# Performance work log

Hardware: AMD Instinct MI355X
Metric: run time of the kernel (lower is better)

Reference implementation:

```python
import jax, jax.numpy as jnp
import numpy as np

FG_THRESH = 0.5  # fg_iou_thresh in RetinaNetLoss.__init__
BG_THRESH = 0.4  # bg_iou_thresh
BELOW_LOW_QUALITY = -1
BETWEEN_THRESHOLDS = -2


def _make_boxes(key, lead_shape, img_size=800.0, max_wh=128.0):
    # Build valid xyxy boxes (x1<x2, y1<y2) inside an img_size image.
    k1, k2 = jax.random.split(key)
    cxcy = jax.random.uniform(k1, lead_shape + (2,), minval=0.0, maxval=img_size)
    wh = jax.random.uniform(k2, lead_shape + (2,), minval=8.0, maxval=max_wh)
    return jnp.concatenate([cxcy - wh * 0.5, cxcy + wh * 0.5], axis=-1)


def setup_inputs() -> dict:
    key = jax.random.key(0)
    kb, ka = jax.random.split(key)
    B, G, A = 8, 64, 120000
    gt_boxes = _make_boxes(kb, (B, G))                 # [B, G, 4] per-image gt boxes
    anchors = _make_boxes(ka, (A,), max_wh=256.0)      # [A, 4] shared anchors
    return {"gt_boxes": gt_boxes, "anchors": anchors}


def _box_iou(boxes1, boxes2):
    # boxes1 [G,4], boxes2 [A,4] -> IoU [G,A] (torchvision box_ops.box_iou)
    area1 = (boxes1[:, 2] - boxes1[:, 0]) * (boxes1[:, 3] - boxes1[:, 1])  # [G]
    area2 = (boxes2[:, 2] - boxes2[:, 0]) * (boxes2[:, 3] - boxes2[:, 1])  # [A]
    lt = jnp.maximum(boxes1[:, None, :2], boxes2[None, :, :2])  # [G,A,2]
    rb = jnp.minimum(boxes1[:, None, 2:], boxes2[None, :, 2:])  # [G,A,2]
    wh = jnp.clip(rb - lt, 0.0)
    inter = wh[..., 0] * wh[..., 1]  # [G,A]
    return inter / (area1[:, None] + area2[None, :] - inter)


def _match(quality):
    # torchvision Matcher(0.5, 0.4, allow_low_quality_matches=True) on quality [G,A]
    matched_vals = quality.max(axis=0)                      # [A] best IoU per anchor
    all_matches = jnp.argmax(quality, axis=0)               # [A] pre-threshold matches
    matches = jnp.where(matched_vals < BG_THRESH, BELOW_LOW_QUALITY, all_matches)
    matches = jnp.where((matched_vals >= BG_THRESH) & (matched_vals < FG_THRESH),
                        BETWEEN_THRESHOLDS, matches)
    # low-quality match recovery: anchors achieving the per-gt max keep their match
    highest_per_gt = quality.max(axis=1, keepdims=True)     # [G,1]
    pred_update = (quality == highest_per_gt).any(axis=0)   # [A]
    matches = jnp.where(pred_update, all_matches, matches)
    return matches.astype(jnp.int64), matched_vals


def reference(gt_boxes, anchors):
    # gt_boxes [B,G,4], anchors [A,4] -> matched_idxs [B,A] int64, matched_vals [B,A]
    def per_image(boxes):
        return _match(_box_iou(boxes, anchors))
    matched_idxs, matched_vals = jax.vmap(per_image)(gt_boxes)
    return matched_idxs, matched_vals
```

## Files before the change

kernel.cpp:

```cpp
#include <hip/hip_runtime.h>


static constexpr int G = 64;

__device__ __forceinline__ float opaque(float x) {
    asm volatile("" : "+v"(x));
    return x;
}

__device__ __forceinline__ int vindex(int i) {
    asm volatile("" : "+v"(i));
    return i;
}

__device__ __forceinline__ float box_area(float x1, float y1, float x2, float y2) {
    return opaque(__fmul_rn(__fsub_rn(x2, x1), __fsub_rn(y2, y1)));
}

__device__ __forceinline__ float inter_area(float gx1, float gy1, float gx2, float gy2,
                                            float ax1, float ay1, float ax2, float ay2) {
    float ltx = fmaxf(gx1, ax1);
    float lty = fmaxf(gy1, ay1);
    float rbx = fminf(gx2, ax2);
    float rby = fminf(gy2, ay2);
    float w = fmaxf(__fsub_rn(rbx, ltx), 0.0f);
    float h = fmaxf(__fsub_rn(rby, lty), 0.0f);
    return opaque(__fmul_rn(w, h));
}

__device__ __forceinline__ float div_rn(float n, float d) {
    float r = __builtin_amdgcn_rcpf(d);
    float e = fmaf(-d, r, 1.0f);
    r = fmaf(e, r, r);
    float q = __fmul_rn(n, r);
    float s = fmaf(-d, q, n);
    q = fmaf(s, r, q);
    s = fmaf(-d, q, n);
    q = fmaf(s, r, q);
    return q;
}

#define DPP_MAX_STAGE(x, ctrl)                                                   \
    do {                                                                         \
        int _yi = __builtin_amdgcn_update_dpp(__float_as_int(x),                 \
                                              __float_as_int(x), (ctrl),         \
                                              0xf, 0xf, false);                  \
        (x) = fmaxf((x), __int_as_float(_yi));                                   \
    } while (0)

__device__ __forceinline__ float wave_max_lane63(float x) {
    DPP_MAX_STAGE(x, 0xB1);
    DPP_MAX_STAGE(x, 0x4E);
    DPP_MAX_STAGE(x, 0x141);
    DPP_MAX_STAGE(x, 0x140);
    DPP_MAX_STAGE(x, 0x142);
    DPP_MAX_STAGE(x, 0x143);
    return x;
}

__global__ void k_init(const float* __restrict__ gt, unsigned int* __restrict__ hpg,
                       float* __restrict__ gab, int BG) {
    int i = blockIdx.x * 256 + threadIdx.x;
    if (i < BG) {
        hpg[i] = 0u;
        float4 gb = ((const float4*)gt)[i];
        gab[i] = box_area(gb.x, gb.y, gb.z, gb.w);
    }
}

template <bool STORE>
__global__ __launch_bounds__(256, 4)
void pass1_k(const float* __restrict__ gt,
             const float* __restrict__ anchors,
             const float* __restrict__ gab,
             unsigned int* __restrict__ hpg,
             unsigned int* __restrict__ sredg,
             float* __restrict__ vmaxA,
             int* __restrict__ amaxA,
             int A, int nchunks) {
    const int b = blockIdx.y;
    const int t = threadIdx.x;

    __shared__ unsigned int sred[G];
    if (t < G) sred[t] = 0u;
    __syncthreads();

    const int base = blockIdx.x * 1024;
    float ax1[4], ay1[4], ax2[4], ay2[4], aar[4];
    bool val[4];
#pragma unroll
    for (int k = 0; k < 4; ++k) {
        int a = base + k * 256 + t;
        val[k] = (a < A);
        float4 ab = ((const float4*)anchors)[val[k] ? a : 0];
        ax1[k] = val[k] ? ab.x : -3.0e38f;
        ay1[k] = val[k] ? ab.y : -3.0e38f;
        ax2[k] = val[k] ? ab.z : -3.0e38f;
        ay2[k] = val[k] ? ab.w : -3.0e38f;
        aar[k] = box_area(ax1[k], ay1[k], ax2[k], ay2[k]);
    }

    const float4* gtb = (const float4*)gt + (size_t)b * G;
    const float* gas = gab + b * G;

    float vmax[4] = {0.0f, 0.0f, 0.0f, 0.0f};
    int amax[4] = {0, 0, 0, 0};

#pragma unroll 8
    for (int g = 0; g < G; ++g) {
        const int gv = vindex(g);
        const float4 gb = gtb[gv];
        const float ga = gas[gv];
        float m = 0.0f;
#pragma unroll
        for (int k = 0; k < 4; ++k) {
            float inter = inter_area(gb.x, gb.y, gb.z, gb.w,
                                     ax1[k], ay1[k], ax2[k], ay2[k]);
            float denom = __fsub_rn(__fadd_rn(ga, aar[k]), inter);
            float q = div_rn(inter, denom);
            if constexpr (STORE) {
                if (q > vmax[k]) { vmax[k] = q; amax[k] = g; }
            }
            m = fmaxf(m, q);
        }
        m = wave_max_lane63(m);
        if ((t & 63) == 63)
            atomicMax(&sred[g], __float_as_uint(m));
    }

    if constexpr (STORE) {
#pragma unroll
        for (int k = 0; k < 4; ++k) {
            if (!val[k]) continue;
            size_t idx = (size_t)b * A + (base + k * 256 + t);
            vmaxA[idx] = vmax[k];
            amaxA[idx] = amax[k];
        }
    }

    __syncthreads();
    if (t < G) {
        atomicMax(&hpg[b * G + t], sred[t]);
        if constexpr (STORE)
            sredg[(size_t)(b * nchunks + blockIdx.x) * G + t] = sred[t];
    }
}

__global__ __launch_bounds__(256, 8)
void pass2_lite(const float* __restrict__ gt,
                const float* __restrict__ anchors,
                const float* __restrict__ gab,
                const unsigned int* __restrict__ hpg,
                const unsigned int* __restrict__ sredg,
                const float* __restrict__ vmaxA,
                const int* __restrict__ amaxA,
                float* __restrict__ out_idx,
                float* __restrict__ out_val,
                int A, int nchunks) {
    const int b = blockIdx.y;
    const int t = threadIdx.x;
    const int base = blockIdx.x * 1024;

    const unsigned int* sb = sredg + (size_t)(b * nchunks + blockIdx.x) * G;
    const unsigned int* hb = hpg + b * G;

    unsigned long long E = 0ull;
#pragma unroll 16
    for (int g = 0; g < G; ++g)
        E |= (sb[g] == hb[g]) ? (1ull << g) : 0ull;

    bool pu[4] = {false, false, false, false};

    if (E != 0ull) {
        const float4* gtb = (const float4*)gt + (size_t)b * G;
        const float* gas = gab + b * G;
        float ax1[4], ay1[4], ax2[4], ay2[4], aar[4];
#pragma unroll
        for (int k = 0; k < 4; ++k) {
            int a = base + k * 256 + t;
            bool v = (a < A);
            float4 ab = ((const float4*)anchors)[v ? a : 0];
            ax1[k] = v ? ab.x : -3.0e38f;
            ay1[k] = v ? ab.y : -3.0e38f;
            ax2[k] = v ? ab.z : -3.0e38f;
            ay2[k] = v ? ab.w : -3.0e38f;
            aar[k] = box_area(ax1[k], ay1[k], ax2[k], ay2[k]);
        }
        unsigned long long e = E;
        while (e) {
            int g = __builtin_ctzll(e);
            e &= e - 1;
            float4 gb = gtb[g];
            float ga = gas[g];
            float hgf = __uint_as_float(hb[g]);
#pragma unroll
            for (int k = 0; k < 4; ++k) {
                float inter = inter_area(gb.x, gb.y, gb.z, gb.w,
                                         ax1[k], ay1[k], ax2[k], ay2[k]);
                float denom = __fsub_rn(__fadd_rn(ga, aar[k]), inter);
                float q = div_rn(inter, denom);
                pu[k] = pu[k] | (q == hgf);
            }
        }
    }

#pragma unroll
    for (int k = 0; k < 4; ++k) {
        int a = base + k * 256 + t;
        if (a >= A) continue;
        size_t idx = (size_t)b * A + a;
        float vm = vmaxA[idx];
        int am = amaxA[idx];
        int m;
        if (pu[k]) {
            m = am;
        } else if (vm < 0.4f) {
            m = -1;
        } else if (vm < 0.5f) {
            m = -2;
        } else {
            m = am;
        }
        out_idx[idx] = (float)m;
        out_val[idx] = vm;
    }
}

__global__ __launch_bounds__(256, 8)
void pass2_match(const float* __restrict__ gt,
                 const float* __restrict__ anchors,
                 const float* __restrict__ gab,
                 const unsigned int* __restrict__ hpg,
                 float* __restrict__ out_idx,
                 float* __restrict__ out_val, int A) {
    const int b = blockIdx.y;
    const int t = threadIdx.x;
    const int base = blockIdx.x * 512;

    float ax1[2], ay1[2], ax2[2], ay2[2], aar[2];
    bool val[2];
#pragma unroll
    for (int k = 0; k < 2; ++k) {
        int a = base + k * 256 + t;
        val[k] = (a < A);
        float4 ab = ((const float4*)anchors)[val[k] ? a : 0];
        ax1[k] = ab.x; ay1[k] = ab.y; ax2[k] = ab.z; ay2[k] = ab.w;
        aar[k] = box_area(ab.x, ab.y, ab.z, ab.w);
    }

    const float4* gtb = (const float4*)gt + (size_t)b * G;
    const float* gas = gab + b * G;
    const unsigned int* hpgb = hpg + b * G;

    float vmax[2] = {0.0f, 0.0f};
    int amax[2] = {0, 0};
    bool pu[2] = {false, false};
#pragma unroll 8
    for (int g = 0; g < G; ++g) {
        float4 gb = gtb[g];
        float ga = gas[g];
        float hg = __uint_as_float(hpgb[g]);
#pragma unroll
        for (int k = 0; k < 2; ++k) {
            float inter = inter_area(gb.x, gb.y, gb.z, gb.w,
                                     ax1[k], ay1[k], ax2[k], ay2[k]);
            float denom = __fsub_rn(__fadd_rn(ga, aar[k]), inter);
            float q = div_rn(inter, denom);
            pu[k] = pu[k] | (q == hg);
            if (q > vmax[k]) { vmax[k] = q; amax[k] = g; }
        }
    }

#pragma unroll
    for (int k = 0; k < 2; ++k) {
        if (!val[k]) continue;
        int m;
        if (pu[k]) m = amax[k];
        else if (vmax[k] < 0.4f) m = -1;
        else if (vmax[k] < 0.5f) m = -2;
        else m = amax[k];
        size_t o = (size_t)b * A + (base + k * 256 + t);
        out_idx[o] = (float)m;
        out_val[o] = vmax[k];
    }
}

extern "C" void kernel_launch(void* const* d_in, const int* in_sizes, int n_in,
                              void* d_out, int out_size, void* d_ws, size_t ws_size,
                              hipStream_t stream) {
    const float* gt = (const float*)d_in[0];
    const float* anchors = (const float*)d_in[1];
    const int BG = in_sizes[0] / 4;
    const int B = BG / G;
    const int A = in_sizes[1] / 4;

    const int nchunks = (A + 1023) / 1024;

    unsigned int* ws = (unsigned int*)d_ws;
    unsigned int* hpg = ws;
    float* gab = (float*)(ws + 512);
    unsigned int* sredg = ws + 1024;
    size_t voff = 1024 + (size_t)nchunks * B * G;
    float* vmaxA = (float*)(ws + voff);
    int* amaxA = (int*)(vmaxA + (size_t)B * A);
    const size_t need = (voff + 2 * (size_t)B * A) * 4;
    const bool fused = (ws_size >= need);

    float* out_idx = (float*)d_out;
    float* out_val = out_idx + (size_t)B * A;

    k_init<<<(BG + 255) / 256, 256, 0, stream>>>(gt, hpg, gab, BG);

    dim3 g1(nchunks, B);
    if (fused) {
        pass1_k<true><<<g1, 256, 0, stream>>>(gt, anchors, gab, hpg, sredg,
                                              vmaxA, amaxA, A, nchunks);
        pass2_lite<<<g1, 256, 0, stream>>>(gt, anchors, gab, hpg, sredg,
                                           vmaxA, amaxA, out_idx, out_val,
                                           A, nchunks);
    } else {
        pass1_k<false><<<g1, 256, 0, stream>>>(gt, anchors, gab, hpg, sredg,
                                               vmaxA, amaxA, A, nchunks);
        dim3 g2((A + 511) / 512, B);
        pass2_match<<<g2, 256, 0, stream>>>(gt, anchors, gab, hpg,
                                            out_idx, out_val, A);
    }
}
```

Measured before the change: 76.11 us.

## Split gt dimension across blocks and merge per-anchor max via packed 64-bit atomics

Pass 1 now splits the 64 gt boxes into two halves along a new grid dimension, doubling the block count, and raises the occupancy hint. Each half-block produces a partial per-anchor max and argmax. These partials are merged with a 64-bit atomicMax on a key that packs the IoU bits with the inverted index, so ties resolve to the lowest gt index. This requires an extra memset of the packed buffer and per-anchor global atomics, in exchange for more parallelism and a single 8-byte load in pass 2.

After: 87.18 us. 14.5% more time.

```diff
diff --git a/kernel.cpp b/kernel.cpp
--- a/kernel.cpp
+++ b/kernel.cpp
@@ -69,20 +69,20 @@
 }
 
 template <bool STORE>
-__global__ __launch_bounds__(256, 4)
+__global__ __launch_bounds__(256, 8)
 void pass1_k(const float* __restrict__ gt,
              const float* __restrict__ anchors,
              const float* __restrict__ gab,
              unsigned int* __restrict__ hpg,
              unsigned int* __restrict__ sredg,
-             float* __restrict__ vmaxA,
-             int* __restrict__ amaxA,
+             unsigned long long* __restrict__ packed,
              int A, int nchunks) {
-    const int b = blockIdx.y;
+    const int b = blockIdx.z;
+    const int g0 = blockIdx.y * 32;
     const int t = threadIdx.x;
 
-    __shared__ unsigned int sred[G];
-    if (t < G) sred[t] = 0u;
+    __shared__ unsigned int sred[32];
+    if (t < 32) sred[t] = 0u;
     __syncthreads();
 
     const int base = blockIdx.x * 1024;
@@ -104,10 +104,11 @@
     const float* gas = gab + b * G;
 
     float vmax[4] = {0.0f, 0.0f, 0.0f, 0.0f};
-    int amax[4] = {0, 0, 0, 0};
+    int amax[4] = {g0, g0, g0, g0};
 
 #pragma unroll 8
-    for (int g = 0; g < G; ++g) {
+    for (int gg = 0; gg < 32; ++gg) {
+        const int g = g0 + gg;
         const int gv = vindex(g);
         const float4 gb = gtb[gv];
         const float ga = gas[gv];
@@ -125,7 +126,7 @@
         }
         m = wave_max_lane63(m);
         if ((t & 63) == 63)
-            atomicMax(&sred[g], __float_as_uint(m));
+            atomicMax(&sred[gg], __float_as_uint(m));
     }
 
     if constexpr (STORE) {
@@ -133,16 +134,19 @@
         for (int k = 0; k < 4; ++k) {
             if (!val[k]) continue;
             size_t idx = (size_t)b * A + (base + k * 256 + t);
-            vmaxA[idx] = vmax[k];
-            amaxA[idx] = amax[k];
+            unsigned long long key =
+                ((unsigned long long)__float_as_uint(vmax[k]) << 32) |
+                (unsigned int)(~amax[k]);
+            atomicMax(&packed[idx], key);
         }
     }
 
     __syncthreads();
-    if (t < G) {
-        atomicMax(&hpg[b * G + t], sred[t]);
+    if (t < 32) {
+        atomicMax(&hpg[b * G + g0 + t], sred[t]);
         if constexpr (STORE)
-            sredg[(size_t)(b * nchunks + blockIdx.x) * G + t] = sred[t];
+            sredg[(size_t)((b * nchunks + blockIdx.x) * 2 + blockIdx.y) * 32 + t]
+                = sred[t];
     }
 }
 
@@ -152,8 +156,7 @@
                 const float* __restrict__ gab,
                 const unsigned int* __restrict__ hpg,
                 const unsigned int* __restrict__ sredg,
-                const float* __restrict__ vmaxA,
-                const int* __restrict__ amaxA,
+                const unsigned long long* __restrict__ packed,
                 float* __restrict__ out_idx,
                 float* __restrict__ out_val,
                 int A, int nchunks) {
@@ -161,7 +164,8 @@
     const int t = threadIdx.x;
     const int base = blockIdx.x * 1024;
 
-    const unsigned int* sb = sredg + (size_t)(b * nchunks + blockIdx.x) * G;
+    const unsigned int* sb =
+        sredg + (size_t)(b * nchunks + blockIdx.x) * 2 * 32;
     const unsigned int* hb = hpg + b * G;
 
     unsigned long long E = 0ull;
@@ -209,8 +213,9 @@
         int a = base + k * 256 + t;
         if (a >= A) continue;
         size_t idx = (size_t)b * A + a;
-        float vm = vmaxA[idx];
-        int am = amaxA[idx];
+        unsigned long long p = packed[idx];
+        float vm = __uint_as_float((unsigned int)(p >> 32));
+        int am = (int)(~(unsigned int)p);
         int m;
         if (pu[k]) {
             m = am;
@@ -300,10 +305,10 @@
     unsigned int* hpg = ws;
     float* gab = (float*)(ws + 512);
     unsigned int* sredg = ws + 1024;
-    size_t voff = 1024 + (size_t)nchunks * B * G;
-    float* vmaxA = (float*)(ws + voff);
-    int* amaxA = (int*)(vmaxA + (size_t)B * A);
-    const size_t need = (voff + 2 * (size_t)B * A) * 4;
+    size_t poff = 1024 + (size_t)nchunks * B * G;
+    poff = (poff + 1) & ~(size_t)1;
+    unsigned long long* packed = (unsigned long long*)(ws + poff);
+    const size_t need = (poff + 2 * (size_t)B * A) * 4;
     const bool fused = (ws_size >= need);
 
     float* out_idx = (float*)d_out;
@@ -311,18 +316,20 @@
 
     k_init<<<(BG + 255) / 256, 256, 0, stream>>>(gt, hpg, gab, BG);
 
-    dim3 g1(nchunks, B);
+    dim3 g1(nchunks, 2, B);
     if (fused) {
+        hipMemsetAsync(packed, 0, (size_t)B * A * 8, stream);
         pass1_k<true><<<g1, 256, 0, stream>>>(gt, anchors, gab, hpg, sredg,
-                                              vmaxA, amaxA, A, nchunks);
-        pass2_lite<<<g1, 256, 0, stream>>>(gt, anchors, gab, hpg, sredg,
-                                           vmaxA, amaxA, out_idx, out_val,
+                                              packed, A, nchunks);
+        dim3 g2(nchunks, B);
+        pass2_lite<<<g2, 256, 0, stream>>>(gt, anchors, gab, hpg, sredg,
+                                           packed, out_idx, out_val,
                                            A, nchunks);
     } else {
         pass1_k<false><<<g1, 256, 0, stream>>>(gt, anchors, gab, hpg, sredg,
-                                               vmaxA, amaxA, A, nchunks);
-        dim3 g2((A + 511) / 512, B);
-        pass2_match<<<g2, 256, 0, stream>>>(gt, anchors, gab, hpg,
-                                            out_idx, out_val, A);
-    }
-}
+                                               packed, A, nchunks);
+        dim3 g2f((A + 511) / 512, B);
+        pass2_match<<<g2f, 256, 0, stream>>>(gt, anchors, gab, hpg,
+                                             out_idx, out_val, A);
+    }
+}
```

## Spatially bin anchors and skip IoU division for wavefronts with no intersection

Applied to the files above, without the earlier changes.

Adds a histogram, scan and scatter pre-pass that sorts anchors into a 16x16 grid of cells by box center, so each wavefront in the matching pass covers spatially nearby anchors. In pass1, intersections are computed first, and the division, argmax and wave reduction are skipped when no lane in the wave intersects the current gt box. pass2 writes results back through a permutation index to restore the original anchor order. The cost is several extra kernel launches, atomics in the scatter, and non-coalesced scattered output writes. The fallback path when workspace is too small now also uses the storing pass1 and appears unsafe.

New measurement: 193.9 us. 155% more time.

```diff
diff --git a/kernel.cpp b/kernel.cpp
--- a/kernel.cpp
+++ b/kernel.cpp
@@ -2,6 +2,7 @@
 
 
 static constexpr int G = 64;
+static constexpr int NCELL = 256;
 
 __device__ __forceinline__ float opaque(float x) {
     asm volatile("" : "+v"(x));
@@ -66,6 +67,51 @@
         float4 gb = ((const float4*)gt)[i];
         gab[i] = box_area(gb.x, gb.y, gb.z, gb.w);
     }
+}
+
+__device__ __forceinline__ int cell_of(float4 ab) {
+    float cx = (ab.x + ab.z) * 0.5f;
+    float cy = (ab.y + ab.w) * 0.5f;
+    int cxi = (int)(cx * 0.02f); cxi = cxi < 0 ? 0 : (cxi > 15 ? 15 : cxi);
+    int cyi = (int)(cy * 0.02f); cyi = cyi < 0 ? 0 : (cyi > 15 ? 15 : cyi);
+    return cyi * 16 + cxi;
+}
+
+__global__ void k_cell(const float* __restrict__ anchors,
+                       unsigned int* __restrict__ hist, int A) {
+    int a = blockIdx.x * 256 + threadIdx.x;
+    if (a >= A) return;
+    atomicAdd(&hist[cell_of(((const float4*)anchors)[a])], 1u);
+}
+
+__global__ void k_scan(const unsigned int* __restrict__ hist,
+                       unsigned int* __restrict__ offs) {
+    __shared__ unsigned int s[NCELL];
+    int t = threadIdx.x;
+    unsigned int v = hist[t];
+    s[t] = v;
+    __syncthreads();
+    for (int d = 1; d < NCELL; d <<= 1) {
+        unsigned int add = (t >= d) ? s[t - d] : 0u;
+        __syncthreads();
+        s[t] += add;
+        __syncthreads();
+    }
+    offs[t] = s[t] - v;
+}
+
+__global__ void k_scatter(const float* __restrict__ anchors,
+                          const unsigned int* __restrict__ offs,
+                          unsigned int* __restrict__ cursor,
+                          float* __restrict__ sortedA,
+                          int* __restrict__ orig, int A) {
+    int a = blockIdx.x * 256 + threadIdx.x;
+    if (a >= A) return;
+    float4 ab = ((const float4*)anchors)[a];
+    int c = cell_of(ab);
+    unsigned int pos = offs[c] + atomicAdd(&cursor[c], 1u);
+    ((float4*)sortedA)[pos] = ab;
+    orig[pos] = a;
 }
 
 template <bool STORE>
@@ -106,26 +152,33 @@
     float vmax[4] = {0.0f, 0.0f, 0.0f, 0.0f};
     int amax[4] = {0, 0, 0, 0};
 
-#pragma unroll 8
+#pragma unroll 4
     for (int g = 0; g < G; ++g) {
         const int gv = vindex(g);
         const float4 gb = gtb[gv];
         const float ga = gas[gv];
-        float m = 0.0f;
-#pragma unroll
-        for (int k = 0; k < 4; ++k) {
-            float inter = inter_area(gb.x, gb.y, gb.z, gb.w,
-                                     ax1[k], ay1[k], ax2[k], ay2[k]);
-            float denom = __fsub_rn(__fadd_rn(ga, aar[k]), inter);
-            float q = div_rn(inter, denom);
-            if constexpr (STORE) {
-                if (q > vmax[k]) { vmax[k] = q; amax[k] = g; }
+        float inter[4];
+#pragma unroll
+        for (int k = 0; k < 4; ++k)
+            inter[k] = inter_area(gb.x, gb.y, gb.z, gb.w,
+                                  ax1[k], ay1[k], ax2[k], ay2[k]);
+        float itest = fmaxf(fmaxf(inter[0], inter[1]),
+                            fmaxf(inter[2], inter[3]));
+        if (__any(itest > 0.0f)) {
+            float m = 0.0f;
+#pragma unroll
+            for (int k = 0; k < 4; ++k) {
+                float denom = __fsub_rn(__fadd_rn(ga, aar[k]), inter[k]);
+                float q = div_rn(inter[k], denom);
+                if constexpr (STORE) {
+                    if (q > vmax[k]) { vmax[k] = q; amax[k] = g; }
+                }
+                m = fmaxf(m, q);
             }
-            m = fmaxf(m, q);
-        }
-        m = wave_max_lane63(m);
-        if ((t & 63) == 63)
-            atomicMax(&sred[g], __float_as_uint(m));
+            m = wave_max_lane63(m);
+            if ((t & 63) == 63)
+                atomicMax(&sred[g], __float_as_uint(m));
+        }
     }
 
     if constexpr (STORE) {
@@ -146,6 +199,7 @@
     }
 }
 
+template <bool SCATTER>
 __global__ __launch_bounds__(256, 8)
 void pass2_lite(const float* __restrict__ gt,
                 const float* __restrict__ anchors,
@@ -154,6 +208,7 @@
                 const unsigned int* __restrict__ sredg,
                 const float* __restrict__ vmaxA,
                 const int* __restrict__ amaxA,
+                const int* __restrict__ orig,
                 float* __restrict__ out_idx,
                 float* __restrict__ out_val,
                 int A, int nchunks) {
@@ -221,67 +276,9 @@
         } else {
             m = am;
         }
-        out_idx[idx] = (float)m;
-        out_val[idx] = vm;
-    }
-}
-
-__global__ __launch_bounds__(256, 8)
-void pass2_match(const float* __restrict__ gt,
-                 const float* __restrict__ anchors,
-                 const float* __restrict__ gab,
-                 const unsigned int* __restrict__ hpg,
-                 float* __restrict__ out_idx,
-                 float* __restrict__ out_val, int A) {
-    const int b = blockIdx.y;
-    const int t = threadIdx.x;
-    const int base = blockIdx.x * 512;
-
-    float ax1[2], ay1[2], ax2[2], ay2[2], aar[2];
-    bool val[2];
-#pragma unroll
-    for (int k = 0; k < 2; ++k) {
-        int a = base + k * 256 + t;
-        val[k] = (a < A);
-        float4 ab = ((const float4*)anchors)[val[k] ? a : 0];
-        ax1[k] = ab.x; ay1[k] = ab.y; ax2[k] = ab.z; ay2[k] = ab.w;
-        aar[k] = box_area(ab.x, ab.y, ab.z, ab.w);
-    }
-
-    const float4* gtb = (const float4*)gt + (size_t)b * G;
-    const float* gas = gab + b * G;
-    const unsigned int* hpgb = hpg + b * G;
-
-    float vmax[2] = {0.0f, 0.0f};
-    int amax[2] = {0, 0};
-    bool pu[2] = {false, false};
-#pragma unroll 8
-    for (int g = 0; g < G; ++g) {
-        float4 gb = gtb[g];
-        float ga = gas[g];
-        float hg = __uint_as_float(hpgb[g]);
-#pragma unroll
-        for (int k = 0; k < 2; ++k) {
-            float inter = inter_area(gb.x, gb.y, gb.z, gb.w,
-                                     ax1[k], ay1[k], ax2[k], ay2[k]);
-            float denom = __fsub_rn(__fadd_rn(ga, aar[k]), inter);
-            float q = div_rn(inter, denom);
-            pu[k] = pu[k] | (q == hg);
-            if (q > vmax[k]) { vmax[k] = q; amax[k] = g; }
-        }
-    }
-
-#pragma unroll
-    for (int k = 0; k < 2; ++k) {
-        if (!val[k]) continue;
-        int m;
-        if (pu[k]) m = amax[k];
-        else if (vmax[k] < 0.4f) m = -1;
-        else if (vmax[k] < 0.5f) m = -2;
-        else m = amax[k];
-        size_t o = (size_t)b * A + (base + k * 256 + t);
+        size_t o = SCATTER ? ((size_t)b * A + orig[a]) : idx;
         out_idx[o] = (float)m;
-        out_val[o] = vmax[k];
+        out_val[o] = vm;
     }
 }
 
@@ -299,12 +296,17 @@
     unsigned int* ws = (unsigned int*)d_ws;
     unsigned int* hpg = ws;
     float* gab = (float*)(ws + 512);
-    unsigned int* sredg = ws + 1024;
-    size_t voff = 1024 + (size_t)nchunks * B * G;
+    unsigned int* hist = ws + 1024;
+    unsigned int* cursor = ws + 1280;
+    unsigned int* offs = ws + 1536;
+    float* sortedA = (float*)(ws + 1792);
+    int* orig = (int*)(ws + 1792 + 4 * (size_t)A);
+    unsigned int* sredg = ws + 1792 + 5 * (size_t)A;
+    size_t voff = 1792 + 5 * (size_t)A + (size_t)nchunks * B * G;
     float* vmaxA = (float*)(ws + voff);
     int* amaxA = (int*)(vmaxA + (size_t)B * A);
     const size_t need = (voff + 2 * (size_t)B * A) * 4;
-    const bool fused = (ws_size >= need);
+    const bool sorted = (ws_size >= need);
 
     float* out_idx = (float*)d_out;
     float* out_val = out_idx + (size_t)B * A;
@@ -312,17 +314,22 @@
     k_init<<<(BG + 255) / 256, 256, 0, stream>>>(gt, hpg, gab, BG);
 
     dim3 g1(nchunks, B);
-    if (fused) {
+    if (sorted) {
+        hipMemsetAsync(hist, 0, 512 * 4, stream);
+        k_cell<<<(A + 255) / 256, 256, 0, stream>>>(anchors, hist, A);
+        k_scan<<<1, NCELL, 0, stream>>>(hist, offs);
+        k_scatter<<<(A + 255) / 256, 256, 0, stream>>>(anchors, offs, cursor,
+                                                       sortedA, orig, A);
+        pass1_k<true><<<g1, 256, 0, stream>>>(gt, sortedA, gab, hpg, sredg,
+                                              vmaxA, amaxA, A, nchunks);
+        pass2_lite<true><<<g1, 256, 0, stream>>>(gt, sortedA, gab, hpg, sredg,
+                                                 vmaxA, amaxA, orig,
+                                                 out_idx, out_val, A, nchunks);
+    } else {
         pass1_k<true><<<g1, 256, 0, stream>>>(gt, anchors, gab, hpg, sredg,
                                               vmaxA, amaxA, A, nchunks);
-        pass2_lite<<<g1, 256, 0, stream>>>(gt, anchors, gab, hpg, sredg,
-                                           vmaxA, amaxA, out_idx, out_val,
-                                           A, nchunks);
-    } else {
-        pass1_k<false><<<g1, 256, 0, stream>>>(gt, anchors, gab, hpg, sredg,
-                                               vmaxA, amaxA, A, nchunks);
-        dim3 g2((A + 511) / 512, B);
-        pass2_match<<<g2, 256, 0, stream>>>(gt, anchors, gab, hpg,
-                                            out_idx, out_val, A);
-    }
-}
+        pass2_lite<false><<<g1, 256, 0, stream>>>(gt, anchors, gab, hpg, sredg,
+                                                  vmaxA, amaxA, orig,
+                                                  out_idx, out_val, A, nchunks);
+    }
+}
```
